# Optimization experiments

Hardware: AMD Instinct MI355X
Metric: run time of the kernel (lower is better)

The kernel has to match this reference:

```python
import jax, jax.numpy as jnp
import numpy as np

FMIN = jnp.finfo(jnp.float32).min
TOPK = 64
RECENT = 128

def rmsnorm(x, w, eps=1e-6):
    return x * jax.lax.rsqrt(jnp.mean(jnp.square(x), axis=-1, keepdims=True) + eps) * w

def sinusoidal_positions(n, d):
    pos = np.arange(n)[:, None].astype(np.float32)
    i = np.arange(d // 2)[None, :].astype(np.float32)
    ang = pos / np.power(10000.0, 2.0 * i / d)
    pe = np.zeros((n, d), np.float32)
    pe[:, 0::2] = np.sin(ang)
    pe[:, 1::2] = np.cos(ang)
    return jnp.asarray(pe)

def _forward(tokens, lengths, query, comp_wv, comp_bv, comp_ww, comp_bw, comp_pos, comp_norm_w,
             idx_qd_w, idx_qd_b, idx_qu_w, idx_qu_b, idx_k_w, idx_k_b, idx_hw_w, idx_hw_b,
             idx_qn_w, idx_kn_w, pool_latents, pool_q_w, pool_q_b, pool_k_w, pool_k_b,
             pool_v_w, pool_v_b, pool_norm_w):
    B, T, D = tokens.shape
    BS = comp_pos.shape[0]
    NB = T // BS  # T chosen divisible by block_size, so no padding branch
    H = idx_hw_w.shape[1]
    IDX = idx_qd_w.shape[1]
    pad_mask = jnp.arange(T)[None, :] >= lengths[:, None]  # True = padded

    # ---- recent window (gather last RECENT valid tokens) ----
    cl = jnp.clip(lengths, 0, T)
    start = jnp.maximum(cl - RECENT, 0)
    pos = jnp.minimum(start[:, None] + jnp.arange(RECENT)[None, :], T - 1)
    recent = jnp.take_along_axis(tokens, pos[:, :, None], axis=1)  # [B,R,D]
    rmask = jnp.arange(RECENT)[None, :] >= jnp.minimum(cl, RECENT)[:, None]
    recent = (recent + sinusoidal_positions(RECENT, D)[None]) * (~rmask)[..., None]

    # ---- learned block compression ----
    blocks = tokens.reshape(B, NB, BS, D)
    bmask = pad_mask.reshape(B, NB, BS)
    values = blocks @ comp_wv + comp_bv
    logits = blocks @ comp_ww + comp_bw + comp_pos  # [B,NB,BS,D]
    logits = jnp.where(bmask[..., None], FMIN, logits)
    w = jax.nn.softmax(logits.astype(jnp.float32), axis=2).astype(values.dtype)
    w = w * (~bmask)[..., None].astype(values.dtype)
    w = w / jnp.maximum(w.sum(axis=2, keepdims=True), jnp.finfo(values.dtype).eps)
    bt = rmsnorm((w * values).sum(axis=2), comp_norm_w)  # [B,NB,D]
    bpm = bmask.all(axis=2)
    bt = bt * (~bpm)[..., None].astype(bt.dtype)

    # ---- sparse top-k block selection ----
    ql = rmsnorm(query @ idx_qd_w + idx_qd_b, idx_qn_w)  # [B,IDX]
    qh = (ql @ idx_qu_w + idx_qu_b).reshape(B, H, IDX)
    keys = rmsnorm(bt @ idx_k_w + idx_k_b, idx_kn_w)  # [B,NB,IDX]
    sbh = jax.nn.relu(jnp.einsum('bhi,bni->bhn', qh, keys))
    hw = jax.nn.softmax(query @ idx_hw_w + idx_hw_b, axis=-1)[:, :, None]
    scores = jnp.where(bpm, FMIN, (sbh * hw).sum(axis=1))
    _, idxs = jax.lax.top_k(scores, TOPK)  # [B,K]
    sel = jnp.take_along_axis(bt, idxs[:, :, None], axis=1)
    sel_mask = jnp.take_along_axis(bpm, idxs, axis=1)

    # ---- global masked-mean token ----
    valid = (~pad_mask).astype(tokens.dtype)
    gtok = (tokens * valid[..., None]).sum(axis=1) / jnp.maximum(valid.sum(axis=1, keepdims=True), 1.0)
    gmask = pad_mask.all(axis=1, keepdims=True)

    src = jnp.concatenate([recent, sel, gtok[:, None]], axis=1)  # [B,N,D]
    smask = jnp.concatenate([rmask, sel_mask, gmask], axis=1)

    # ---- target-aware latent cross-attention pooling ----
    v = (~smask)[..., None].astype(src.dtype)
    mt = src * v
    lq = pool_latents[None] + (query @ pool_q_w + pool_q_b)[:, None]  # [B,L,D]
    k = mt @ pool_k_w + pool_k_b
    vv = (mt @ pool_v_w + pool_v_b) * v
    sc = jnp.einsum('bld,bnd->bln', lq, k) * (D ** -0.5)
    safe = smask & ~smask.all(axis=-1, keepdims=True)  # avoid all-masked softmax rows
    sc = jnp.where(safe[:, None], FMIN, sc)
    pw = jax.nn.softmax(sc.astype(jnp.float32), axis=-1).astype(vv.dtype)
    lat = jnp.einsum('bln,bnd->bld', pw, vv)
    all_pad = smask.all(axis=1, keepdims=True)  # [B,1]
    lat = rmsnorm(lat, pool_norm_w) * (~all_pad)[..., None].astype(lat.dtype)
    return lat  # [B,L,D]

def setup_inputs() -> dict:
    key = jax.random.key(0)
    ks = jax.random.split(key, 16)
    B, T, D, BS, H, IDX, L = 8, 8192, 512, 32, 8, 64, 16
    def n(k, shape, s=0.02):
        return jax.random.normal(k, shape, jnp.float32) * s
    return {
        'tokens': jax.random.normal(ks[0], (B, T, D), jnp.float32),
        'lengths': jax.random.randint(ks[1], (B,), 1, T + 1, jnp.int32),
        'query': jax.random.normal(ks[2], (B, D), jnp.float32),
        'comp_wv': n(ks[3], (D, D)), 'comp_bv': jnp.zeros(D),
        'comp_ww': n(ks[4], (D, D)), 'comp_bw': jnp.zeros(D),
        'comp_pos': jnp.zeros((BS, D)),
        'comp_norm_w': jnp.ones(D),
        'idx_qd_w': n(ks[5], (D, IDX)), 'idx_qd_b': jnp.zeros(IDX),
        'idx_qu_w': n(ks[6], (IDX, H * IDX)), 'idx_qu_b': jnp.zeros(H * IDX),
        'idx_k_w': n(ks[7], (D, IDX)), 'idx_k_b': jnp.zeros(IDX),
        'idx_hw_w': n(ks[8], (D, H)), 'idx_hw_b': jnp.zeros(H),
        'idx_qn_w': jnp.ones(IDX), 'idx_kn_w': jnp.ones(IDX),
        'pool_latents': n(ks[9], (L, D)),
        'pool_q_w': n(ks[10], (D, D)), 'pool_q_b': jnp.zeros(D),
        'pool_k_w': n(ks[11], (D, D)), 'pool_k_b': jnp.zeros(D),
        'pool_v_w': n(ks[12], (D, D)), 'pool_v_b': jnp.zeros(D),
        'pool_norm_w': jnp.ones(D),
    }

def reference(tokens, lengths, query, comp_wv, comp_bv, comp_ww, comp_bw, comp_pos, comp_norm_w,
              idx_qd_w, idx_qd_b, idx_qu_w, idx_qu_b, idx_k_w, idx_k_b, idx_hw_w, idx_hw_b,
              idx_qn_w, idx_kn_w, pool_latents, pool_q_w, pool_q_b, pool_k_w, pool_k_b,
              pool_v_w, pool_v_b, pool_norm_w):
    return _forward(tokens, lengths, query, comp_wv, comp_bv, comp_ww, comp_bw, comp_pos, comp_norm_w,
                    idx_qd_w, idx_qd_b, idx_qu_w, idx_qu_b, idx_k_w, idx_k_b, idx_hw_w, idx_hw_b,
                    idx_qn_w, idx_kn_w, pool_latents, pool_q_w, pool_q_b, pool_k_w, pool_k_b,
                    pool_v_w, pool_v_b, pool_norm_w)
```

## Files before the change

### kernel.cpp

```cpp
#include <hip/hip_runtime.h>
#include <stdint.h>

typedef __attribute__((ext_vector_type(8))) _Float16 half8;
typedef __attribute__((ext_vector_type(8))) short short8;
typedef __attribute__((ext_vector_type(4))) float f32x4;

#define FMIN_F (-3.4028234663852886e38f)

__device__ __forceinline__ unsigned short rne_bf16(float x) {
  unsigned u = __float_as_uint(x);
  unsigned r = (u + 0x7FFFu + ((u >> 16) & 1u)) >> 16;
  return (unsigned short)r;
}

__device__ __forceinline__ void split16(float x, unsigned short& h, unsigned short& l) {
  _Float16 hh = (_Float16)x;
  float r = x - (float)hh;
  _Float16 ll = (_Float16)r;
  union { _Float16 f; unsigned short u; } a, b;
  a.f = hh; b.f = ll;
  h = a.u; l = b.u;
}

__device__ __forceinline__ void glds16(const unsigned short* g, unsigned short* l) {
  __builtin_amdgcn_global_load_lds(
      (const __attribute__((address_space(1))) unsigned int*)g,
      (__attribute__((address_space(3))) unsigned int*)l, 16, 0, 0);
}

__global__ __launch_bounds__(256) void k_split(const float* __restrict__ tok,
    const int* __restrict__ lengths, int row0, unsigned short* __restrict__ A2,
    float* __restrict__ gpart) {
  __shared__ float ps[512];
  int wg = blockIdx.x, tid = threadIdx.x;
  int colv = tid & 127;
  int rh = tid >> 7;
  int r0 = wg << 4;
  int b0 = (row0 + r0) >> 13;
  int part = wg & 511;
  int len = lengths[b0];
  float sx = 0.f, sy = 0.f, sz = 0.f, sw = 0.f;
#pragma unroll
  for (int i = 0; i < 8; ++i) {
    int lrow = r0 + (i << 1) + rh;
    int grow = row0 + lrow;
    const float4 v = ((const float4*)(tok + (size_t)grow * 512))[colv];
    ushort4 oh, ol;
    split16(v.x, oh.x, ol.x); split16(v.y, oh.y, ol.y);
    split16(v.z, oh.z, ol.z); split16(v.w, oh.w, ol.w);
    *(ushort4*)(A2 + (size_t)lrow * 1024 + colv * 4) = oh;
    *(ushort4*)(A2 + (size_t)lrow * 1024 + 512 + colv * 4) = ol;
    if ((grow & 8191) < len) { sx += v.x; sy += v.y; sz += v.z; sw += v.w; }
  }
  if (rh == 0) {
    ps[colv * 4 + 0] = sx; ps[colv * 4 + 1] = sy;
    ps[colv * 4 + 2] = sz; ps[colv * 4 + 3] = sw;
  }
  __syncthreads();
  if (rh == 1) {
    ps[colv * 4 + 0] += sx; ps[colv * 4 + 1] += sy;
    ps[colv * 4 + 2] += sz; ps[colv * 4 + 3] += sw;
  }
  __syncthreads();
  float* gp = gpart + ((size_t)b0 * 512 + part) * 512;
  gp[tid] = ps[tid];
  gp[tid + 256] = ps[tid + 256];
}

__global__ __launch_bounds__(256) void k_gred(const float* __restrict__ gpart,
    float* __restrict__ gsum) {
  int b = blockIdx.x, tid = threadIdx.x;
  float a0 = 0.f, a1 = 0.f;
  for (int part = 0; part < 512; ++part) {
    const float* gp = gpart + ((size_t)b * 512 + part) * 512;
    a0 += gp[tid];
    a1 += gp[tid + 256];
  }
  gsum[b * 512 + tid] = a0;
  gsum[b * 512 + tid + 256] = a1;
}

__global__ __launch_bounds__(256) void k_wsplit(const float* __restrict__ wv,
    const float* __restrict__ ww, unsigned short* __restrict__ W2) {
  __shared__ float t[64][65];
  int kk0 = blockIdx.x * 64, d0 = blockIdx.y * 64, m = blockIdx.z;
  const float* W = m ? ww : wv;
  int tid = threadIdx.x;
  for (int i = tid; i < 4096; i += 256) {
    int k = i >> 6, d = i & 63;
    t[k][d] = W[(size_t)(kk0 + k) * 512 + d0 + d];
  }
  __syncthreads();
  int dr = tid >> 2, kq = tid & 3;
  int d = d0 + dr;
  int n = (d >> 5) * 64 + m * 32 + (d & 31);
  size_t baseH = (size_t)n * 1024 + kk0 + kq * 16;
  for (int q = 0; q < 16; ++q) {
    unsigned short hh, ll;
    split16(t[kq * 16 + q][dr], hh, ll);
    W2[baseH + q] = hh;
    W2[baseH + 512 + q] = ll;
  }
}

__global__ __launch_bounds__(256) void k_wpool(const float* __restrict__ wk,
    const float* __restrict__ wv, unsigned short* __restrict__ PW) {
  __shared__ float t[64][65];
  int kk0 = blockIdx.x * 64, d0 = blockIdx.y * 64, m = blockIdx.z;
  const float* W = m ? wv : wk;
  int tid = threadIdx.x;
  for (int i = tid; i < 4096; i += 256) {
    int k = i >> 6, d = i & 63;
    t[k][d] = W[(size_t)(kk0 + k) * 512 + d0 + d];
  }
  __syncthreads();
  int dr = tid >> 2, kq = tid & 3;
  int n = m * 512 + d0 + dr;
  size_t base = (size_t)n * 512 + kk0 + kq * 16;
  for (int q = 0; q < 16; ++q)
    PW[base + q] = rne_bf16(t[kq * 16 + q][dr]);
}

__global__ __launch_bounds__(256) void k_gemm128(
    const unsigned short* __restrict__ A2, const unsigned short* __restrict__ W2,
    const float* __restrict__ bv, const float* __restrict__ bw,
    const float* __restrict__ cpos, const int* __restrict__ lengths,
    int row0, float* __restrict__ ctx) {
  __shared__ __align__(16) unsigned short Ash[128 * 64];
  __shared__ __align__(16) unsigned short Asl[128 * 64];
  __shared__ __align__(16) unsigned short Bsh[128 * 64];
  __shared__ __align__(16) unsigned short Bsl[128 * 64];
  __shared__ float pos_s[32 * 64];
  int mt = blockIdx.x, ny = blockIdx.y;
  int tid = threadIdx.x;
  int wave = tid >> 6, lane = tid & 63;
  int m0 = mt << 7, n0 = ny << 7;
  for (int i = tid; i < 2048; i += 256) {
    int s = i >> 6, c = i & 63;
    pos_s[i] = cpos[s * 512 + ny * 64 + c];
  }
  f32x4 acc[4][4];
#pragma unroll
  for (int i = 0; i < 4; ++i)
#pragma unroll
    for (int j = 0; j < 4; ++j) acc[i][j] = (f32x4){0.f, 0.f, 0.f, 0.f};
  int lrow = lane >> 3, lcol = lane & 7;
  int wm = wave >> 1, wn = wave & 1;
  int l15 = lane & 15, lg4 = lane >> 4;
  int scs_ = (lcol ^ lrow) * 8;
  int rx = (l15 & 7);
  for (int kk = 0; kk < 8; ++kk) {
    int k0 = kk << 6;
#pragma unroll
    for (int j = 0; j < 4; ++j) {
      int r = wave * 32 + j * 8 + lrow;
      size_t ga = (size_t)(m0 + r) * 1024 + k0 + scs_;
      size_t gb = (size_t)(n0 + r) * 1024 + k0 + scs_;
      int ls = r * 64 + lcol * 8;
      glds16(A2 + ga, Ash + ls);
      glds16(A2 + ga + 512, Asl + ls);
      glds16(W2 + gb, Bsh + ls);
      glds16(W2 + gb + 512, Bsl + ls);
    }
    __syncthreads();
#pragma unroll
    for (int ks = 0; ks < 2; ++ks) {
      int cofs = ((ks * 4 + lg4) ^ rx) * 8;
      half8 bh[4], bl[4];
#pragma unroll
      for (int i = 0; i < 4; ++i) {
        bh[i] = *(const half8*)(Bsh + (wn * 64 + i * 16 + l15) * 64 + cofs);
        bl[i] = *(const half8*)(Bsl + (wn * 64 + i * 16 + l15) * 64 + cofs);
      }
#pragma unroll
      for (int mi = 0; mi < 4; ++mi) {
        half8 ah = *(const half8*)(Ash + (wm * 64 + mi * 16 + l15) * 64 + cofs);
        half8 al = *(const half8*)(Asl + (wm * 64 + mi * 16 + l15) * 64 + cofs);
#pragma unroll
        for (int ni = 0; ni < 4; ++ni) {
          acc[mi][ni] = __builtin_amdgcn_mfma_f32_16x16x32_f16(ah, bh[ni], acc[mi][ni], 0, 0, 0);
          acc[mi][ni] = __builtin_amdgcn_mfma_f32_16x16x32_f16(al, bh[ni], acc[mi][ni], 0, 0, 0);
          acc[mi][ni] = __builtin_amdgcn_mfma_f32_16x16x32_f16(ah, bl[ni], acc[mi][ni], 0, 0, 0);
        }
      }
    }
    __syncthreads();
  }
  int bidx = (row0 + m0) >> 13;
  int len = lengths[bidx];
#pragma unroll
  for (int niv = 0; niv < 2; ++niv) {
    int d = (ny * 2 + wn) * 32 + niv * 16 + l15;
    int dloc = wn * 32 + niv * 16 + l15;
    float bwv = bw[d], bvv = bv[d];
#pragma unroll
    for (int blk = 0; blk < 2; ++blk) {
      int growL = m0 + wm * 64 + blk * 32;
      int nb = ((row0 + growL) & 8191) >> 5;
      int vcnt = min(max(len - nb * 32, 0), 32);
      float lg[8], vl[8];
      float mx = FMIN_F;
#pragma unroll
      for (int j = 0; j < 8; ++j) {
        int mi = blk * 2 + (j >> 2);
        int r = j & 3;
        int s = ((j >> 2) << 4) + lg4 * 4 + r;
        float L = acc[mi][2 + niv][r] + bwv + pos_s[s * 64 + dloc];
        float V = acc[mi][niv][r] + bvv;
        lg[j] = L; vl[j] = V;
        if (s < vcnt) mx = fmaxf(mx, L);
      }
      mx = fmaxf(mx, __shfl_xor(mx, 16));
      mx = fmaxf(mx, __shfl_xor(mx, 32));
      float num = 0.f, den = 0.f;
#pragma unroll
      for (int j = 0; j < 8; ++j) {
        int s = ((j >> 2) << 4) + lg4 * 4 + (j & 3);
        if (s < vcnt) {
          float e = __expf(lg[j] - mx);
          num += e * vl[j];
          den += e;
        }
      }
      num += __shfl_xor(num, 16); num += __shfl_xor(num, 32);
      den += __shfl_xor(den, 16); den += __shfl_xor(den, 32);
      float o = (den > 0.f) ? (num / den) : 0.f;
      if (lg4 == 0)
        ctx[((size_t)bidx * 256 + nb) * 512 + d] = o;
    }
  }
}

__global__ __launch_bounds__(64) void k_btk(const float* __restrict__ ctx,
    const float* __restrict__ nw, const float* __restrict__ kw,
    const float* __restrict__ kb, const float* __restrict__ knw,
    float* __restrict__ bt, float* __restrict__ keys) {
  int row = blockIdx.x, lane = threadIdx.x;
  __shared__ float bs[512];
  const float* cp = ctx + (size_t)row * 512 + lane * 8;
  float x[8];
#pragma unroll
  for (int j = 0; j < 8; ++j) x[j] = cp[j];
  float ss = 0.f;
#pragma unroll
  for (int j = 0; j < 8; ++j) ss += x[j] * x[j];
#pragma unroll
  for (int o = 1; o < 64; o <<= 1) ss += __shfl_xor(ss, o);
  float sc = rsqrtf(ss * (1.f / 512.f) + 1e-6f);
  float* op = bt + (size_t)row * 512 + lane * 8;
  const float* nwp = nw + lane * 8;
#pragma unroll
  for (int j = 0; j < 8; ++j) {
    float y = x[j] * sc * nwp[j];
    op[j] = y;
    bs[lane * 8 + j] = y;
  }
  __syncthreads();
  float a = kb[lane];
  for (int k = 0; k < 512; ++k) a += bs[k] * kw[k * 64 + lane];
  float s2 = a * a;
#pragma unroll
  for (int o = 1; o < 64; o <<= 1) s2 += __shfl_xor(s2, o);
  keys[(size_t)row * 64 + lane] = a * rsqrtf(s2 * (1.f / 64.f) + 1e-6f) * knw[lane];
}

__global__ __launch_bounds__(256) void k_sel(
    const float* __restrict__ query, const float* __restrict__ keys,
    const int* __restrict__ lengths,
    const float* __restrict__ qdw, const float* __restrict__ qdb,
    const float* __restrict__ quw, const float* __restrict__ qub,
    const float* __restrict__ hww, const float* __restrict__ hwb,
    const float* __restrict__ qnw, int* __restrict__ idxs) {
  int b = blockIdx.x, tid = threadIdx.x;
  __shared__ float qs[512], qls[64], qhs[512], hws[8], scs[256];
  __shared__ float ks_s[256 * 65];
  int wave = tid >> 6, lane = tid & 63;
  {
    const float* kb_g = keys + (size_t)b * 256 * 64;
    for (int r = wave; r < 256; r += 4)
      ks_s[r * 65 + lane] = kb_g[r * 64 + lane];
  }
  for (int i = tid; i < 512; i += 256) qs[i] = query[b * 512 + i];
  __syncthreads();
  if (tid < 64) {
    float a = qdb[tid];
    for (int k = 0; k < 512; ++k) a += qs[k] * qdw[k * 64 + tid];
    float ss = a * a;
#pragma unroll
    for (int o = 1; o < 64; o <<= 1) ss += __shfl_xor(ss, o);
    qls[tid] = a * rsqrtf(ss * (1.f / 64.f) + 1e-6f) * qnw[tid];
  }
  __syncthreads();
  for (int j = tid; j < 512; j += 256) {
    float a = qub[j];
    for (int k = 0; k < 64; ++k) a += qls[k] * quw[k * 512 + j];
    qhs[j] = a;
  }
  if (tid < 8) {
    float a = hwb[tid];
    for (int k = 0; k < 512; ++k) a += qs[k] * hww[k * 8 + tid];
    hws[tid] = a;
  }
  __syncthreads();
  if (tid == 0) {
    float m = hws[0];
    for (int h = 1; h < 8; ++h) m = fmaxf(m, hws[h]);
    float s = 0.f, e[8];
    for (int h = 0; h < 8; ++h) { e[h] = __expf(hws[h] - m); s += e[h]; }
    for (int h = 0; h < 8; ++h) hws[h] = e[h] / s;
  }
  __syncthreads();
  {
    int len = lengths[b];
    int n = tid;
    float sc = FMIN_F;
    if (n * 32 < len) {
      sc = 0.f;
      const float* kr = ks_s + n * 65;
      for (int h = 0; h < 8; ++h) {
        float dp = 0.f;
#pragma unroll
        for (int i = 0; i < 64; ++i) dp += qhs[h * 64 + i] * kr[i];
        sc += fmaxf(dp, 0.f) * hws[h];
      }
    }
    scs[n] = sc;
  }
  __syncthreads();
  if (tid < 64) {
    unsigned long long kk[4];
#pragma unroll
    for (int j = 0; j < 4; ++j) {
      int n = j * 64 + tid;
      unsigned u = __float_as_uint(scs[n]);
      u = (u & 0x80000000u) ? ~u : (u | 0x80000000u);
      kk[j] = ((unsigned long long)u << 32) | (unsigned long long)(255 - n);
    }
    for (int r = 0; r < 64; ++r) {
      unsigned long long m = kk[0];
      if (kk[1] > m) m = kk[1];
      if (kk[2] > m) m = kk[2];
      if (kk[3] > m) m = kk[3];
#pragma unroll
      for (int o = 1; o < 64; o <<= 1) {
        unsigned long long t = __shfl_xor(m, o);
        if (t > m) m = t;
      }
      if (tid == 0) idxs[b * 64 + r] = 255 - (int)(m & 0xFFull);
#pragma unroll
      for (int j = 0; j < 4; ++j) if (kk[j] == m) kk[j] = 0ull;
    }
  }
}

__global__ __launch_bounds__(128) void k_src(const float* __restrict__ tok,
    const float* __restrict__ bt, const float* __restrict__ gsum,
    const int* __restrict__ lengths, const int* __restrict__ idxs,
    unsigned short* __restrict__ src_bf, int* __restrict__ smask) {
  int b = blockIdx.x, n = blockIdx.y, tid = threadIdx.x;
  int d0 = tid * 4;
  if (n >= 193) {
    size_t prow = 1544 + (size_t)b * 15 + (n - 193);
    ushort4 z; z.x = 0; z.y = 0; z.z = 0; z.w = 0;
    *(ushort4*)(src_bf + prow * 512 + d0) = z;
    return;
  }
  int len = lengths[b];
  float v0 = 0.f, v1 = 0.f, v2 = 0.f, v3 = 0.f;
  int sm = 0;
  if (n < 128) {
    int cl = min(max(len, 0), 8192);
    int start = max(cl - 128, 0);
    int pos = min(start + n, 8191);
    bool vis = n < min(cl, 128);
    sm = vis ? 0 : 1;
    if (vis) {
      const float* tp = tok + ((size_t)b * 8192 + pos) * 512 + d0;
      float pn = (float)n;
#pragma unroll
      for (int j = 0; j < 4; ++j) {
        int d = d0 + j;
        int i = d >> 1;
        float ang = pn * __expf(-9.210340371976184f * ((float)i * (1.f / 256.f)));
        float pe = (d & 1) ? cosf(ang) : sinf(ang);
        float t = tp[j] + pe;
        if (j == 0) v0 = t; else if (j == 1) v1 = t; else if (j == 2) v2 = t; else v3 = t;
      }
    }
  } else if (n < 192) {
    int idx = idxs[b * 64 + (n - 128)];
    sm = (idx * 32 >= len) ? 1 : 0;
    const float* bp = bt + ((size_t)b * 256 + idx) * 512 + d0;
    v0 = bp[0]; v1 = bp[1]; v2 = bp[2]; v3 = bp[3];
  } else {
    sm = 0;
    float inv = 1.f / (float)max(len, 1);
    const float* gp = gsum + b * 512 + d0;
    v0 = gp[0] * inv; v1 = gp[1] * inv; v2 = gp[2] * inv; v3 = gp[3] * inv;
  }
  ushort4 o;
  o.x = rne_bf16(v0); o.y = rne_bf16(v1); o.z = rne_bf16(v2); o.w = rne_bf16(v3);
  *(ushort4*)(src_bf + ((size_t)b * 193 + n) * 512 + d0) = o;
  if (tid == 0) smask[b * 193 + n] = sm;
}

__global__ __launch_bounds__(256) void k_kvm(
    const unsigned short* __restrict__ src_bf, const unsigned short* __restrict__ PW,
    float* __restrict__ kv) {
  __shared__ __align__(16) unsigned short As[128 * 64];
  __shared__ __align__(16) unsigned short Bs[128 * 64];
  int m0 = blockIdx.x << 7, n0 = blockIdx.y << 7;
  int tid = threadIdx.x;
  int wave = tid >> 6, lane = tid & 63;
  int wm = wave >> 1, wn = wave & 1;
  int l15 = lane & 15, lg4 = lane >> 4;
  int lrow = lane >> 3, lcol = lane & 7;
  f32x4 acc[4][4];
#pragma unroll
  for (int i = 0; i < 4; ++i)
#pragma unroll
    for (int j = 0; j < 4; ++j) acc[i][j] = (f32x4){0.f, 0.f, 0.f, 0.f};
  for (int kk = 0; kk < 8; ++kk) {
    int k0 = kk << 6;
#pragma unroll
    for (int j = 0; j < 4; ++j) {
      int r = wave * 32 + j * 8 + lrow;
      glds16(src_bf + (size_t)(m0 + r) * 512 + k0 + lcol * 8, As + r * 64 + lcol * 8);
      glds16(PW + (size_t)(n0 + r) * 512 + k0 + lcol * 8, Bs + r * 64 + lcol * 8);
    }
    __syncthreads();
#pragma unroll
    for (int ks = 0; ks < 2; ++ks) {
      int kb = ks * 32 + lg4 * 8;
      short8 av[4], bf[4];
#pragma unroll
      for (int i = 0; i < 4; ++i) {
        av[i] = *(const short8*)(As + (wm * 64 + i * 16 + l15) * 64 + kb);
        bf[i] = *(const short8*)(Bs + (wn * 64 + i * 16 + l15) * 64 + kb);
      }
#pragma unroll
      for (int mi = 0; mi < 4; ++mi)
#pragma unroll
        for (int ni = 0; ni < 4; ++ni)
          acc[mi][ni] = __builtin_amdgcn_mfma_f32_16x16x32_bf16(av[mi], bf[ni], acc[mi][ni], 0, 0, 0);
    }
    __syncthreads();
  }
#pragma unroll
  for (int mi = 0; mi < 4; ++mi)
#pragma unroll
    for (int ni = 0; ni < 4; ++ni)
#pragma unroll
      for (int rr = 0; rr < 4; ++rr) {
        int grow = m0 + wm * 64 + mi * 16 + lg4 * 4 + rr;
        kv[(size_t)grow * 1024 + n0 + wn * 64 + ni * 16 + l15] = acc[mi][ni][rr];
      }
}

__global__ __launch_bounds__(256) void k_qproj(const float* __restrict__ query,
    const float* __restrict__ pqw, const float* __restrict__ pqb,
    float* __restrict__ qp) {
  int b = blockIdx.x;
  int c = blockIdx.y * 256 + threadIdx.x;
  __shared__ float qs[512];
  for (int i = threadIdx.x; i < 512; i += 256) qs[i] = query[b * 512 + i];
  __syncthreads();
  float a = pqb[c];
  for (int k = 0; k < 512; ++k) a += qs[k] * pqw[(size_t)k * 512 + c];
  qp[b * 512 + c] = a;
}

__global__ __launch_bounds__(256) void k_attn(const float* __restrict__ kv,
    const float* __restrict__ qproj, const float* __restrict__ latents,
    const float* __restrict__ pkb, const float* __restrict__ pvb,
    const float* __restrict__ pnw, const int* __restrict__ smask,
    float* __restrict__ out) {
  int b = blockIdx.x, l = blockIdx.y, tid = threadIdx.x;
  int wave = tid >> 6, lane = tid & 63;
  __shared__ float lq_s[512];
  __shared__ float w_s[256];
  __shared__ float red_s[256];
  __shared__ int sm_s[256];
  for (int i = tid; i < 512; i += 256) lq_s[i] = latents[l * 512 + i] + qproj[b * 512 + i];
  sm_s[tid] = (tid < 193) ? smask[b * 193 + tid] : 1;
  w_s[tid] = FMIN_F;
  __syncthreads();
  red_s[tid] = (tid < 193 && sm_s[tid]) ? 1.f : 0.f;
  __syncthreads();
  for (int s = 128; s > 0; s >>= 1) { if (tid < s) red_s[tid] += red_s[tid + s]; __syncthreads(); }
  bool allm = (red_s[0] > 192.5f);
  __syncthreads();
  red_s[tid] = pkb[tid] * lq_s[tid] + pkb[tid + 256] * lq_s[tid + 256];
  __syncthreads();
  for (int s = 128; s > 0; s >>= 1) { if (tid < s) red_s[tid] += red_s[tid + s]; __syncthreads(); }
  float pkbdot = red_s[0];
  __syncthreads();
  for (int n = wave; n < 193; n += 4) {
    const float* kr = kv + ((size_t)b * 193 + n) * 1024 + lane * 8;
    float4 a = *(const float4*)(kr);
    float4 c = *(const float4*)(kr + 4);
    const float* lq = lq_s + lane * 8;
    float dp = a.x * lq[0] + a.y * lq[1] + a.z * lq[2] + a.w * lq[3]
             + c.x * lq[4] + c.y * lq[5] + c.z * lq[6] + c.w * lq[7];
#pragma unroll
    for (int o = 1; o < 64; o <<= 1) dp += __shfl_xor(dp, o);
    if (lane == 0) {
      float sc = (dp + pkbdot) * 0.04419417382415922f;
      if (sm_s[n] && !allm) sc = FMIN_F;
      w_s[n] = sc;
    }
  }
  __syncthreads();
  float sc = w_s[tid];
  red_s[tid] = sc;
  __syncthreads();
  for (int s = 128; s > 0; s >>= 1) { if (tid < s) red_s[tid] = fmaxf(red_s[tid], red_s[tid + s]); __syncthreads(); }
  float mx = red_s[0];
  __syncthreads();
  float e = __expf(sc - mx);
  w_s[tid] = e;
  red_s[tid] = e;
  __syncthreads();
  for (int s = 128; s > 0; s >>= 1) { if (tid < s) red_s[tid] += red_s[tid + s]; __syncthreads(); }
  float invS = 1.f / red_s[0];
  __syncthreads();
  float o0 = 0.f, o1 = 0.f;
  const float* vbase = kv + (size_t)b * 193 * 1024 + 512;
#pragma unroll 4
  for (int n = 0; n < 193; ++n) {
    float w = w_s[n];
    const float* vr = vbase + (size_t)n * 1024;
    o0 += w * vr[tid];
    o1 += w * vr[tid + 256];
  }
  o0 = o0 * invS + pvb[tid];
  o1 = o1 * invS + pvb[tid + 256];
  red_s[tid] = o0 * o0 + o1 * o1;
  __syncthreads();
  for (int s = 128; s > 0; s >>= 1) { if (tid < s) red_s[tid] += red_s[tid + s]; __syncthreads(); }
  float scale = rsqrtf(red_s[0] * (1.f / 512.f) + 1e-6f);
  if (allm) scale = 0.f;
  out[((size_t)b * 16 + l) * 512 + tid] = o0 * scale * pnw[tid];
  out[((size_t)b * 16 + l) * 512 + tid + 256] = o1 * scale * pnw[tid + 256];
}

extern "C" void kernel_launch(void* const* d_in, const int* in_sizes, int n_in,
                              void* d_out, int out_size, void* d_ws, size_t ws_size,
                              hipStream_t stream) {
  (void)in_sizes; (void)n_in; (void)out_size; (void)ws_size;
  const float* tokens      = (const float*)d_in[0];
  const int*   lengths     = (const int*)d_in[1];
  const float* query       = (const float*)d_in[2];
  const float* comp_wv     = (const float*)d_in[3];
  const float* comp_bv     = (const float*)d_in[4];
  const float* comp_ww     = (const float*)d_in[5];
  const float* comp_bw     = (const float*)d_in[6];
  const float* comp_pos    = (const float*)d_in[7];
  const float* comp_norm_w = (const float*)d_in[8];
  const float* idx_qd_w    = (const float*)d_in[9];
  const float* idx_qd_b    = (const float*)d_in[10];
  const float* idx_qu_w    = (const float*)d_in[11];
  const float* idx_qu_b    = (const float*)d_in[12];
  const float* idx_k_w     = (const float*)d_in[13];
  const float* idx_k_b     = (const float*)d_in[14];
  const float* idx_hw_w    = (const float*)d_in[15];
  const float* idx_hw_b    = (const float*)d_in[16];
  const float* idx_qn_w    = (const float*)d_in[17];
  const float* idx_kn_w    = (const float*)d_in[18];
  const float* pool_latents= (const float*)d_in[19];
  const float* pool_q_w    = (const float*)d_in[20];
  const float* pool_q_b    = (const float*)d_in[21];
  const float* pool_k_w    = (const float*)d_in[22];
  const float* pool_k_b    = (const float*)d_in[23];
  const float* pool_v_w    = (const float*)d_in[24];
  const float* pool_v_b    = (const float*)d_in[25];
  const float* pool_norm_w = (const float*)d_in[26];

  char* ws = (char*)d_ws;
  unsigned short* A2    = (unsigned short*)(ws + 0);
  float*          bt    = (float*)(ws + 0);
  float*          keys  = (float*)(ws + 4194304);
  int*            idxs  = (int*)  (ws + 4718592);
  int*            smask = (int*)  (ws + 4720640);
  float*          qproj = (float*)(ws + 4728832);
  unsigned short* PW2   = (unsigned short*)(ws + 4745216);
  unsigned short* src_bf= (unsigned short*)(ws + 5793792);
  float*          kv    = (float*)(ws + 7497728);
  float*          gpart = (float*)(ws + 33554432);
  float*          ctx   = (float*)(ws + 41943040);
  unsigned short* W2    = (unsigned short*)(ws + 46137344);
  float*          gsum  = (float*)(ws + 48234496);

  k_wsplit<<<dim3(8, 8, 2), 256, 0, stream>>>(comp_wv, comp_ww, W2);
  for (int c = 0; c < 4; ++c) {
    int row0 = c * 16384;
    k_split<<<1024, 256, 0, stream>>>(tokens, lengths, row0, A2, gpart);
    k_gemm128<<<dim3(128, 8), 256, 0, stream>>>(A2, W2, comp_bv, comp_bw,
                                                comp_pos, lengths, row0, ctx);
  }
  k_gred<<<8, 256, 0, stream>>>(gpart, gsum);
  k_wpool<<<dim3(8, 8, 2), 256, 0, stream>>>(pool_k_w, pool_v_w, PW2);
  k_btk<<<2048, 64, 0, stream>>>(ctx, comp_norm_w, idx_k_w, idx_k_b, idx_kn_w,
                                 bt, keys);
  k_sel<<<8, 256, 0, stream>>>(query, keys, lengths, idx_qd_w, idx_qd_b,
                               idx_qu_w, idx_qu_b, idx_hw_w, idx_hw_b,
                               idx_qn_w, idxs);
  k_src<<<dim3(8, 208), 128, 0, stream>>>(tokens, bt, gsum, lengths, idxs,
                                          src_bf, smask);
  k_kvm<<<dim3(13, 8), 256, 0, stream>>>(src_bf, PW2, kv);
  k_qproj<<<dim3(8, 2), 256, 0, stream>>>(query, pool_q_w, pool_q_b, qproj);
  k_attn<<<dim3(8, 16), 256, 0, stream>>>(kv, qproj, pool_latents, pool_k_b,
                                          pool_v_b, pool_norm_w, smask,
                                          (float*)d_out);
}
```

Measured before the change: 435.7 us.

## Process all rows in single split and GEMM launches instead of four chunks

Removes the four-chunk loop, so k_split and k_gemm128 each run once over all 65536 rows. The split fp16 hi/lo A2 buffer grows to the full input size, and the gpart, ctx, W2 and gsum workspace offsets move to make room. k_gred is also split over a second grid dimension to double its parallelism. The aim is to cut launch count and tail effects and to fill the GPU with larger grids. The cost is a much larger intermediate buffer that may no longer stay cache-resident between the split and the GEMM.

```diff
diff --git a/kernel.cpp b/kernel.cpp
--- a/kernel.cpp
+++ b/kernel.cpp
@@ -29,28 +29,27 @@
 }
 
 __global__ __launch_bounds__(256) void k_split(const float* __restrict__ tok,
-    const int* __restrict__ lengths, int row0, unsigned short* __restrict__ A2,
+    const int* __restrict__ lengths, unsigned short* __restrict__ A2,
     float* __restrict__ gpart) {
   __shared__ float ps[512];
   int wg = blockIdx.x, tid = threadIdx.x;
   int colv = tid & 127;
   int rh = tid >> 7;
   int r0 = wg << 4;
-  int b0 = (row0 + r0) >> 13;
+  int b0 = r0 >> 13;
   int part = wg & 511;
   int len = lengths[b0];
   float sx = 0.f, sy = 0.f, sz = 0.f, sw = 0.f;
 #pragma unroll
   for (int i = 0; i < 8; ++i) {
-    int lrow = r0 + (i << 1) + rh;
-    int grow = row0 + lrow;
-    const float4 v = ((const float4*)(tok + (size_t)grow * 512))[colv];
+    int row = r0 + (i << 1) + rh;
+    const float4 v = ((const float4*)(tok + (size_t)row * 512))[colv];
     ushort4 oh, ol;
     split16(v.x, oh.x, ol.x); split16(v.y, oh.y, ol.y);
     split16(v.z, oh.z, ol.z); split16(v.w, oh.w, ol.w);
-    *(ushort4*)(A2 + (size_t)lrow * 1024 + colv * 4) = oh;
-    *(ushort4*)(A2 + (size_t)lrow * 1024 + 512 + colv * 4) = ol;
-    if ((grow & 8191) < len) { sx += v.x; sy += v.y; sz += v.z; sw += v.w; }
+    *(ushort4*)(A2 + (size_t)row * 1024 + colv * 4) = oh;
+    *(ushort4*)(A2 + (size_t)row * 1024 + 512 + colv * 4) = ol;
+    if ((row & 8191) < len) { sx += v.x; sy += v.y; sz += v.z; sw += v.w; }
   }
   if (rh == 0) {
     ps[colv * 4 + 0] = sx; ps[colv * 4 + 1] = sy;
@@ -69,15 +68,12 @@
 
 __global__ __launch_bounds__(256) void k_gred(const float* __restrict__ gpart,
     float* __restrict__ gsum) {
-  int b = blockIdx.x, tid = threadIdx.x;
-  float a0 = 0.f, a1 = 0.f;
-  for (int part = 0; part < 512; ++part) {
-    const float* gp = gpart + ((size_t)b * 512 + part) * 512;
-    a0 += gp[tid];
-    a1 += gp[tid + 256];
-  }
-  gsum[b * 512 + tid] = a0;
-  gsum[b * 512 + tid + 256] = a1;
+  int b = blockIdx.x, half = blockIdx.y, tid = threadIdx.x;
+  int c = half * 256 + tid;
+  float a0 = 0.f;
+  for (int part = 0; part < 512; ++part)
+    a0 += gpart[((size_t)b * 512 + part) * 512 + c];
+  gsum[b * 512 + c] = a0;
 }
 
 __global__ __launch_bounds__(256) void k_wsplit(const float* __restrict__ wv,
@@ -125,7 +121,7 @@
     const unsigned short* __restrict__ A2, const unsigned short* __restrict__ W2,
     const float* __restrict__ bv, const float* __restrict__ bw,
     const float* __restrict__ cpos, const int* __restrict__ lengths,
-    int row0, float* __restrict__ ctx) {
+    float* __restrict__ ctx) {
   __shared__ __align__(16) unsigned short Ash[128 * 64];
   __shared__ __align__(16) unsigned short Asl[128 * 64];
   __shared__ __align__(16) unsigned short Bsh[128 * 64];
@@ -186,7 +182,7 @@
     }
     __syncthreads();
   }
-  int bidx = (row0 + m0) >> 13;
+  int bidx = m0 >> 13;
   int len = lengths[bidx];
 #pragma unroll
   for (int niv = 0; niv < 2; ++niv) {
@@ -196,7 +192,7 @@
 #pragma unroll
     for (int blk = 0; blk < 2; ++blk) {
       int growL = m0 + wm * 64 + blk * 32;
-      int nb = ((row0 + growL) & 8191) >> 5;
+      int nb = (growL & 8191) >> 5;
       int vcnt = min(max(len - nb * 32, 0), 32);
       float lg[8], vl[8];
       float mx = FMIN_F;
@@ -586,19 +582,16 @@
   unsigned short* PW2   = (unsigned short*)(ws + 4745216);
   unsigned short* src_bf= (unsigned short*)(ws + 5793792);
   float*          kv    = (float*)(ws + 7497728);
-  float*          gpart = (float*)(ws + 33554432);
-  float*          ctx   = (float*)(ws + 41943040);
-  unsigned short* W2    = (unsigned short*)(ws + 46137344);
-  float*          gsum  = (float*)(ws + 48234496);
+  float*          gpart = (float*)(ws + 134217728);
+  float*          ctx   = (float*)(ws + 142606336);
+  unsigned short* W2    = (unsigned short*)(ws + 146800640);
+  float*          gsum  = (float*)(ws + 148897792);
 
   k_wsplit<<<dim3(8, 8, 2), 256, 0, stream>>>(comp_wv, comp_ww, W2);
-  for (int c = 0; c < 4; ++c) {
-    int row0 = c * 16384;
-    k_split<<<1024, 256, 0, stream>>>(tokens, lengths, row0, A2, gpart);
-    k_gemm128<<<dim3(128, 8), 256, 0, stream>>>(A2, W2, comp_bv, comp_bw,
-                                                comp_pos, lengths, row0, ctx);
-  }
-  k_gred<<<8, 256, 0, stream>>>(gpart, gsum);
+  k_split<<<4096, 256, 0, stream>>>(tokens, lengths, A2, gpart);
+  k_gemm128<<<dim3(512, 8), 256, 0, stream>>>(A2, W2, comp_bv, comp_bw,
+                                              comp_pos, lengths, ctx);
+  k_gred<<<dim3(8, 2), 256, 0, stream>>>(gpart, gsum);
   k_wpool<<<dim3(8, 8, 2), 256, 0, stream>>>(pool_k_w, pool_v_w, PW2);
   k_btk<<<2048, 64, 0, stream>>>(ctx, comp_norm_w, idx_k_w, idx_k_b, idx_kn_w,
                                  bt, keys);
```

Result: slower. 455.5 us (+4.5%).
